# Kernel tuning notes

Measured on AMD Instinct MI355X. Metric: run time of the kernel, lower is better.

Reference implementation:

```python
import jax, jax.numpy as jnp
import numpy as np

D_MODEL = 1024
SEL_DIM = 64
CONFIGS = [(4, 32), (8, 64), (16, 128)]  # (heads, dim)
B, T = 2, 2048


def setup_inputs() -> dict:
    key = jax.random.key(0)
    ks = jax.random.split(key, 20)
    s = 0.02  # init scale for stability
    inp = {
        "x": jax.random.normal(ks[0], (B, T, D_MODEL), jnp.float32),
        "sel_w1": jax.random.normal(ks[1], (SEL_DIM, D_MODEL), jnp.float32) * s,
        "sel_b1": jnp.zeros((SEL_DIM,), jnp.float32),
        "sel_w2": jax.random.normal(ks[2], (SEL_DIM, SEL_DIM), jnp.float32) * s,
        "sel_b2": jnp.zeros((SEL_DIM,), jnp.float32),
        "sel_w3": jax.random.normal(ks[3], (len(CONFIGS), SEL_DIM), jnp.float32) * s,
        "sel_b3": jnp.zeros((len(CONFIGS),), jnp.float32),
    }
    for i, (h, d) in enumerate(CONFIGS):
        inp[f"qw{i}"] = jax.random.normal(ks[4 + 3 * i], (h * d, D_MODEL), jnp.float32) * s
        inp[f"kw{i}"] = jax.random.normal(ks[5 + 3 * i], (d, D_MODEL), jnp.float32) * s
        inp[f"ww{i}"] = jax.random.normal(ks[6 + 3 * i], (h, D_MODEL), jnp.float32) * s
    return inp


def _seq_features(x):
    # x: [b,t,d]
    b, t, d = x.shape
    seq_mean = jnp.mean(x, axis=1, keepdims=True)            # [b,1,d]
    seq_std = jnp.std(x, axis=1, keepdims=True, ddof=1)      # torch.std is unbiased
    pos = (jnp.arange(t, dtype=x.dtype) / t)[None, :, None]  # [1,t,1] broadcast to [b,t,d]
    return x + seq_mean + seq_std + pos * 0.1


def _forward(x, sel_w1, sel_b1, sel_w2, sel_b2, sel_w3, sel_b3,
             qw0, kw0, ww0, qw1, kw1, ww1, qw2, kw2, ww2):
    b, t, dm = x.shape
    feats = _seq_features(x)
    h1 = jax.nn.relu(feats @ sel_w1.T + sel_b1)
    h2 = jax.nn.relu(h1 @ sel_w2.T + sel_b2)
    config_probs = jax.nn.softmax(h2 @ sel_w3.T + sel_b3, axis=-1)  # [b,t,ncfg]

    per_cfg = [(qw0, kw0, ww0), (qw1, kw1, ww1), (qw2, kw2, ww2)]
    final = jnp.zeros((b, t, t), dtype=x.dtype)
    for i, ((heads, dim), (qw, kw, ww)) in enumerate(zip(CONFIGS, per_cfg)):
        q = (x @ qw.T).reshape(b, t, heads, dim)   # [b,t,h,d]
        k = x @ kw.T                               # [b,s,d]
        w = x @ ww.T                               # [b,t,h]
        dots = jnp.einsum('bthd,bsd->bths', q, k)  # [b,t,h,s]
        score = jnp.einsum('bths,bth->bts', jax.nn.relu(dots), w)  # relu*weight, sum heads
        final = final + config_probs[:, :, i:i + 1] * score
    return final


def reference(x, sel_w1, sel_b1, sel_w2, sel_b2, sel_w3, sel_b3,
              qw0, kw0, ww0, qw1, kw1, ww1, qw2, kw2, ww2):
    return _forward(x, sel_w1, sel_b1, sel_w2, sel_b2, sel_w3, sel_b3,
                    qw0, kw0, ww0, qw1, kw1, ww1, qw2, kw2, ww2)
```

## Files before the change

kernel.cpp:

```cpp
#include <hip/hip_runtime.h>
#include <hip/hip_fp16.h>
#include <cstdint>
#include <cstddef>
#include <math.h>

#define B_ 2
#define T_ 2048
#define D_ 1024
#define M_ (B_*T_)

#define QO0 0
#define KO0 128
#define WO0 160
#define QO1 168
#define KO1 680
#define WO1 744
#define QO2 752
#define KO2 2800
#define WO2 2928
#define SELO 2944
#define LDN 3072

typedef float f32x16 __attribute__((ext_vector_type(16)));
typedef short bf16x8 __attribute__((ext_vector_type(8)));
typedef unsigned short u16;

__device__ __forceinline__ u16 f2bf(float f) {
    unsigned int u = __float_as_uint(f);
    unsigned int r = (u + 0x7fffu + ((u >> 16) & 1u)) >> 16;
    return (u16)r;
}
__device__ __forceinline__ float bf2f(u16 b) {
    return __uint_as_float(((unsigned int)b) << 16);
}

__device__ __forceinline__ void gload16(const void* g, void* l) {
    __builtin_amdgcn_global_load_lds(
        (const __attribute__((address_space(1))) unsigned int*)g,
        (__attribute__((address_space(3))) unsigned int*)l,
        16, 0, 0);
}

__device__ __forceinline__ void stage_plane(const u16* src_base, int row_stride, int k0,
                                            int rg, int lane, u16* dst) {
    int rl  = lane >> 2;
    int row = rg * 16 + rl;
    int q   = (lane & 3) ^ (rl & 3) ^ ((rl >> 2) & 3);
    const u16* s = src_base + (size_t)row * row_stride + k0 + q * 8;
    gload16(s, dst + rg * 512);
}

__global__ void stats1(const float* __restrict__ x, float* __restrict__ part,
                       float* __restrict__ part2, u16* __restrict__ Xh) {
    int d  = blockIdx.x * 256 + threadIdx.x;
    int tc = blockIdx.y;
    int b  = blockIdx.z;
    size_t base = (size_t)b * T_ * D_ + (size_t)tc * 16 * D_ + d;
    float s = 0.f, s2 = 0.f;
#pragma unroll
    for (int t = 0; t < 16; ++t) {
        float v = x[base + (size_t)t * D_];
        s += v; s2 += v * v;
        Xh[base + (size_t)t * D_] = f2bf(v);
    }
    part [(b * 128 + tc) * D_ + d] = s;
    part2[(b * 128 + tc) * D_ + d] = s2;
}

__global__ void stats2(const float* __restrict__ part, const float* __restrict__ part2,
                       const float* __restrict__ w1,
                       float* __restrict__ msd, float* __restrict__ s1) {
    __shared__ float msL[1024];
    __shared__ float ps[64][17];
    __shared__ float pw[64][17];
    int b = blockIdx.x, tid = threadIdx.x;
    float s = 0.f, s2 = 0.f;
#pragma unroll 8
    for (int i = 0; i < 128; ++i) {
        s  += part [(b * 128 + i) * D_ + tid];
        s2 += part2[(b * 128 + i) * D_ + tid];
    }
    float mean = s / (float)T_;
    float var  = (s2 - (float)T_ * mean * mean) / (float)(T_ - 1);
    msL[tid] = mean + sqrtf(fmaxf(var, 0.f));
    __syncthreads();
    int j = tid >> 4, cc = tid & 15;
    float am = 0.f, aw = 0.f;
    const float* wr = w1 + (size_t)j * D_ + cc * 64;
    const float* mr = msL + cc * 64;
    for (int dd = 0; dd < 64; ++dd) { float w = wr[dd]; am += mr[dd] * w; aw += w; }
    ps[j][cc] = am; pw[j][cc] = aw;
    __syncthreads();
    if (tid < 64) {
        float sm = 0.f, sw = 0.f;
        for (int i = 0; i < 16; ++i) { sm += ps[tid][i]; sw += pw[tid][i]; }
        msd[b * 64 + tid] = sm;
        if (b == 0) s1[tid] = sw;
    }
}

__global__ void split_w(const float* __restrict__ qw0, const float* __restrict__ kw0,
                        const float* __restrict__ ww0, const float* __restrict__ qw1,
                        const float* __restrict__ kw1, const float* __restrict__ ww1,
                        const float* __restrict__ qw2, const float* __restrict__ kw2,
                        const float* __restrict__ ww2, const float* __restrict__ w1s,
                        u16* __restrict__ Wh) {
    int row = blockIdx.x;
    int col = threadIdx.x * 4;
    const float* src = nullptr;
    if      (row < 128)  src = qw0 + (size_t)row * D_;
    else if (row < 160)  src = kw0 + (size_t)(row - 128) * D_;
    else if (row < 164)  src = ww0 + (size_t)(row - 160) * D_;
    else if (row < 168)  src = nullptr;
    else if (row < 680)  src = qw1 + (size_t)(row - 168) * D_;
    else if (row < 744)  src = kw1 + (size_t)(row - 680) * D_;
    else if (row < 752)  src = ww1 + (size_t)(row - 744) * D_;
    else if (row < 2800) src = qw2 + (size_t)(row - 752) * D_;
    else if (row < 2928) src = kw2 + (size_t)(row - 2800) * D_;
    else if (row < 2944) src = ww2 + (size_t)(row - 2928) * D_;
    else if (row < 3008) src = w1s + (size_t)(row - 2944) * D_;
    float4 v = src ? *(const float4*)(src + col) : make_float4(0.f, 0.f, 0.f, 0.f);
    ushort4 h;
    h.x = f2bf(v.x); h.y = f2bf(v.y); h.z = f2bf(v.z); h.w = f2bf(v.w);
    *(ushort4*)&Wh[(size_t)row * D_ + col] = h;
}

__global__ __launch_bounds__(256, 3) void proj_gemm(
    const u16* __restrict__ Xh, const u16* __restrict__ Wh, u16* __restrict__ Ph) {
    __shared__ u16 As[8192], Bs[8192];
    int tid = threadIdx.x;
    int wave = tid >> 6, lane = tid & 63;
    int bm = blockIdx.x * 128, bn = blockIdx.y * 128;
    int wt = wave >> 1, wn = wave & 1;
    int fm = lane & 31, hv = lane >> 5;
    int tkey = (fm & 3) ^ ((fm >> 2) & 3);
    f32x16 acc[2][2];
#pragma unroll
    for (int i = 0; i < 2; ++i)
#pragma unroll
        for (int j = 0; j < 2; ++j)
#pragma unroll
            for (int r = 0; r < 16; ++r) acc[i][j][r] = 0.f;

    const u16* xh = Xh + (size_t)bm * D_;
    const u16* wh = Wh + (size_t)bn * D_;

    for (int kc = 0; kc < 16; ++kc) {
        int k0 = kc * 64;
#pragma unroll
        for (int i = 0; i < 8; ++i) {
            int j = wave * 8 + i;
            int mat = j >> 4;
            int pl  = (j >> 3) & 1;
            int rg  = j & 7;
            stage_plane(mat ? wh : xh, D_, k0 + pl * 32, rg, lane,
                        (mat ? Bs : As) + pl * 4096);
        }
        __syncthreads();
#pragma unroll
        for (int ks = 0; ks < 4; ++ks) {
            int pl = ks >> 1;
            int slot8 = (((ks & 1) * 2 + hv) ^ tkey) * 8;
            bf16x8 a_h[2], b_h[2];
#pragma unroll
            for (int t = 0; t < 2; ++t) {
                a_h[t] = *(const bf16x8*)&As[pl * 4096 + (wt * 64 + t * 32 + fm) * 32 + slot8];
                b_h[t] = *(const bf16x8*)&Bs[pl * 4096 + (wn * 64 + t * 32 + fm) * 32 + slot8];
            }
#pragma unroll
            for (int ti = 0; ti < 2; ++ti)
#pragma unroll
                for (int tj = 0; tj < 2; ++tj)
                    acc[ti][tj] = __builtin_amdgcn_mfma_f32_32x32x16_bf16(a_h[ti], b_h[tj], acc[ti][tj], 0, 0, 0);
        }
        __syncthreads();
    }
#pragma unroll
    for (int ti = 0; ti < 2; ++ti)
#pragma unroll
        for (int tj = 0; tj < 2; ++tj)
#pragma unroll
            for (int r = 0; r < 16; ++r) {
                int row = bm + wt * 64 + ti * 32 + (r & 3) + 8 * (r >> 2) + 4 * hv;
                int col = bn + wn * 64 + tj * 32 + fm;
                Ph[(size_t)row * LDN + col] = f2bf(acc[ti][tj][r]);
            }
}

__global__ void selector2(const u16* __restrict__ Ph,
                          const float* __restrict__ msd, const float* __restrict__ s1,
                          const float* __restrict__ b1, const float* __restrict__ w2,
                          const float* __restrict__ b2, const float* __restrict__ w3,
                          const float* __restrict__ b3, __half* __restrict__ WP) {
    __shared__ float h1s[4][64];
    __shared__ float h2s[4][64];
    __shared__ float lg[4][3];
    int tid = threadIdx.x;
    int slot = tid >> 6, j = tid & 63;
    int bt = blockIdx.x * 4 + slot;
    int b = bt >> 11, t = bt & 2047;
    size_t pidx = (size_t)bt * LDN + SELO + j;
    float v = bf2f(Ph[pidx])
            + msd[b * 64 + j] + 0.1f * ((float)t / (float)T_) * s1[j] + b1[j];
    h1s[slot][j] = fmaxf(v, 0.f);
    __syncthreads();
    float a2 = b2[j];
#pragma unroll 8
    for (int d = 0; d < 64; ++d) a2 = fmaf(h1s[slot][d], w2[j * 64 + d], a2);
    h2s[slot][j] = fmaxf(a2, 0.f);
    __syncthreads();
    if (j < 3) {
        float a3 = b3[j];
        for (int d = 0; d < 64; ++d) a3 = fmaf(h2s[slot][d], w3[j * 64 + d], a3);
        lg[slot][j] = a3;
    }
    __syncthreads();
    if (j < 28) {
        float m = fmaxf(lg[slot][0], fmaxf(lg[slot][1], lg[slot][2]));
        float e0 = expf(lg[slot][0] - m), e1 = expf(lg[slot][1] - m), e2 = expf(lg[slot][2] - m);
        float inv = 1.f / (e0 + e1 + e2);
        int wcol = (j < 4) ? (WO0 + j) : ((j < 12) ? (WO1 + j - 4) : (WO2 + j - 12));
        float p = ((j < 4) ? e0 : ((j < 12) ? e1 : e2)) * inv;
        float w = bf2f(Ph[(size_t)bt * LDN + wcol]);
        WP[(size_t)(b * 28 + j) * T_ + t] = __float2half(w * p);
    }
}

__device__ __forceinline__ int qcol_of(int c) {
    if (c < 2)  return QO0 + c * 64;
    if (c < 10) return QO1 + (c - 2) * 64;
    return QO2 + (c - 10) * 64;
}

__global__ __launch_bounds__(256, 2) void score_kernel(
    const u16* __restrict__ Ph, const __half* __restrict__ WP, float* __restrict__ out) {
    __shared__ u16 Qs[2][8192];
    __shared__ u16 Ks[4 * 4096];
    __shared__ __half wpL[3584];
    int tid = threadIdx.x;
    int wave = tid >> 6, lane = tid & 63;
    int wt = wave >> 1, wn = wave & 1;
    int fm = lane & 31, hv = lane >> 5;
    int tkey = (fm & 3) ^ ((fm >> 2) & 3);

    int n = blockIdx.z * 256 + blockIdx.y * 16 + blockIdx.x;
    int p = (n & 7) * 4 + (n >> 7);
    int xb = (n >> 3) & 15;
    int b = p >> 4, yb = p & 15;
    int t0 = yb * 128, s0 = xb * 128;

    const u16* Pq = Ph + (size_t)(b * T_ + t0) * LDN;
    const u16* Pk = Ph + (size_t)(b * T_ + s0) * LDN;

    auto stageQ = [&](int buf, int qcol) {
#pragma unroll
        for (int i = 0; i < 4; ++i) {
            int j = (wave << 2) + i;
            int pl = j >> 3, rg = j & 7;
            stage_plane(Pq, LDN, qcol + pl * 32, rg, lane, &Qs[buf][pl * 4096]);
        }
    };

#pragma unroll
    for (int i = 0; i < 6; ++i) {
        int j = i * 4 + wave;
        int pl = j >> 3, rg = j & 7;
        int col = (pl == 0) ? KO0 : ((pl == 1) ? KO1 : KO1 + 32);
        stage_plane(Pk, LDN, col, rg, lane, &Ks[pl * 4096]);
    }
#pragma unroll
    for (int i = 0; i < 2; ++i) {
        int j = i * 4 + wave;
        if (j < 7) {
            const __half* src = WP + (size_t)(b * 28 + j * 4 + (lane >> 4)) * T_ + t0 + (lane & 15) * 8;
            gload16(src, (u16*)wpL + j * 512);
        }
    }
    stageQ(0, QO0);

    f32x16 outacc[2][2], dots[2][2], Z16;
#pragma unroll
    for (int r = 0; r < 16; ++r) Z16[r] = 0.f;
#pragma unroll
    for (int i = 0; i < 2; ++i)
#pragma unroll
        for (int j = 0; j < 2; ++j)
#pragma unroll
            for (int r = 0; r < 16; ++r) { outacc[i][j][r] = 0.f; dots[i][j][r] = 0.f; }

    auto epi = [&](int g) {
#pragma unroll
        for (int ti = 0; ti < 2; ++ti) {
            int rowbase = wt * 64 + ti * 32 + 4 * hv;
#pragma unroll
            for (int rq = 0; rq < 4; ++rq) {
                const __half2* wp2 = (const __half2*)&wpL[g * 128 + rowbase + rq * 8];
                float2 f01 = __half22float2(wp2[0]);
                float2 f23 = __half22float2(wp2[1]);
                float wv[4] = {f01.x, f01.y, f23.x, f23.y};
#pragma unroll
                for (int tj = 0; tj < 2; ++tj)
#pragma unroll
                    for (int r2 = 0; r2 < 4; ++r2) {
                        int r = rq * 4 + r2;
                        outacc[ti][tj][r] += fmaxf(dots[ti][tj][r], 0.f) * wv[r2];
                    }
            }
        }
    };

    auto phase64 = [&](const u16* qb, int kpA, int kpB, bool z0, bool midBreak,
                       int gMid, bool hasEnd, int gEnd) {
#pragma unroll
        for (int ks = 0; ks < 4; ++ks) {
            int kp = (ks < 2) ? kpA : kpB;
            int slot8 = (((ks & 1) * 2 + hv) ^ tkey) * 8;
            bool zero = (ks == 0 && z0) || (ks == 2 && midBreak);
            bf16x8 kf[2], qf[2];
#pragma unroll
            for (int tj = 0; tj < 2; ++tj)
                kf[tj] = *(const bf16x8*)&Ks[kp * 4096 + (wn * 64 + tj * 32 + fm) * 32 + slot8];
#pragma unroll
            for (int ti = 0; ti < 2; ++ti)
                qf[ti] = *(const bf16x8*)&qb[(ks >> 1) * 4096 + (wt * 64 + ti * 32 + fm) * 32 + slot8];
#pragma unroll
            for (int ti = 0; ti < 2; ++ti)
#pragma unroll
                for (int tj = 0; tj < 2; ++tj)
                    dots[ti][tj] = __builtin_amdgcn_mfma_f32_32x32x16_bf16(
                        qf[ti], kf[tj], zero ? Z16 : dots[ti][tj], 0, 0, 0);
            if (ks == 1 && midBreak) epi(gMid);
            if (ks == 3 && hasEnd)   epi(gEnd);
        }
    };

#pragma unroll
    for (int c = 0; c < 2; ++c) {
        __syncthreads();
        stageQ((c + 1) & 1, qcol_of(c + 1));
        phase64(Qs[c & 1], 0, 0, true, true, 2 * c, true, 2 * c + 1);
    }
    for (int h = 0; h < 8; ++h) {
        int c = 2 + h;
        __syncthreads();
        stageQ((c + 1) & 1, qcol_of(c + 1));
        phase64(Qs[c & 1], 1, 2, true, false, -1, true, 4 + h);
        if (h == 7) {
            __syncthreads();
            for (int j = wave; j < 32; j += 4) {
                int pl = j >> 3, rg = j & 7;
                stage_plane(Pk, LDN, KO2 + pl * 32, rg, lane, &Ks[pl * 4096]);
            }
        }
    }
    for (int h = 0; h < 16; ++h) {
        int c = 10 + 2 * h;
        __syncthreads();
        stageQ((c + 1) & 1, qcol_of(c + 1));
        phase64(Qs[c & 1], 0, 1, true, false, -1, false, -1);
        __syncthreads();
        if (c + 1 < 41) stageQ(c & 1, qcol_of(c + 2));
        phase64(Qs[(c + 1) & 1], 2, 3, false, false, -1, true, 12 + h);
    }

#pragma unroll
    for (int ti = 0; ti < 2; ++ti)
#pragma unroll
        for (int tj = 0; tj < 2; ++tj)
#pragma unroll
            for (int r = 0; r < 16; ++r) {
                int trow = wt * 64 + ti * 32 + (r & 3) + 8 * (r >> 2) + 4 * hv;
                int scol = wn * 64 + tj * 32 + fm;
                out[(size_t)(b * T_ + t0 + trow) * T_ + (s0 + scol)] = outacc[ti][tj][r];
            }
}

extern "C" void kernel_launch(void* const* d_in, const int* in_sizes, int n_in,
                              void* d_out, int out_size, void* d_ws, size_t ws_size,
                              hipStream_t stream) {
    const float* x   = (const float*)d_in[0];
    const float* w1  = (const float*)d_in[1];
    const float* b1  = (const float*)d_in[2];
    const float* w2  = (const float*)d_in[3];
    const float* b2  = (const float*)d_in[4];
    const float* w3  = (const float*)d_in[5];
    const float* b3  = (const float*)d_in[6];
    const float* qw0 = (const float*)d_in[7];
    const float* kw0 = (const float*)d_in[8];
    const float* ww0 = (const float*)d_in[9];
    const float* qw1 = (const float*)d_in[10];
    const float* kw1 = (const float*)d_in[11];
    const float* ww1 = (const float*)d_in[12];
    const float* qw2 = (const float*)d_in[13];
    const float* kw2 = (const float*)d_in[14];
    const float* ww2 = (const float*)d_in[15];
    float* out = (float*)d_out;

    float* fb = (float*)d_ws;
    float* PA  = fb; fb += (size_t)B_ * 128 * D_;
    float* PA2 = fb; fb += (size_t)B_ * 128 * D_;
    float* MSD = fb; fb += 128;
    float* S1  = fb; fb += 64;
    __half* WP = (__half*)fb; fb += (size_t)B_ * 28 * T_ / 2;
    u16* ub = (u16*)fb;
    u16* Wh = ub; ub += (size_t)LDN * D_;
    u16* Xh = ub; ub += (size_t)M_ * D_;
    u16* Ph = ub; ub += (size_t)M_ * LDN;

    stats1<<<dim3(D_ / 256, 128, B_), 256, 0, stream>>>(x, PA, PA2, Xh);
    stats2<<<dim3(B_), 1024, 0, stream>>>(PA, PA2, w1, MSD, S1);
    split_w<<<dim3(LDN), 256, 0, stream>>>(qw0, kw0, ww0, qw1, kw1, ww1,
                                           qw2, kw2, ww2, w1, Wh);
    proj_gemm<<<dim3(M_ / 128, LDN / 128), 256, 0, stream>>>(Xh, Wh, Ph);
    selector2<<<dim3(M_ / 4), 256, 0, stream>>>(Ph, MSD, S1, b1, w2, b2, w3, b3, WP);
    score_kernel<<<dim3(T_ / 128, T_ / 128, B_), 256, 0, stream>>>(Ph, WP, out);
}
```

Before: 256.8 us.

## Register-resident K fragments with 128x64 score tiles, split stats2 across blocks

The score kernel now uses 128x64 output tiles instead of 128x128, so each wave owns a 32x64 strip. The K fragments for each config are loaded once into registers rather than re-read from LDS on every step. LDS is unified into one buffer and launch bounds rise to 3 blocks per CU, with 1024 blocks launched. The single-block stats2 reduction is split into two wider parallel kernels (column reduction, then a shuffle-based dot with w1) to remove a serial bottleneck. The trade-offs are higher register pressure, twice as many Q loads per output, and one extra kernel launch.

```diff
diff --git a/kernel.cpp b/kernel.cpp
--- a/kernel.cpp
+++ b/kernel.cpp
@@ -67,35 +67,50 @@
     part2[(b * 128 + tc) * D_ + d] = s2;
 }
 
-__global__ void stats2(const float* __restrict__ part, const float* __restrict__ part2,
-                       const float* __restrict__ w1,
-                       float* __restrict__ msd, float* __restrict__ s1) {
-    __shared__ float msL[1024];
-    __shared__ float ps[64][17];
-    __shared__ float pw[64][17];
-    int b = blockIdx.x, tid = threadIdx.x;
+__global__ void stats2a(const float* __restrict__ part, const float* __restrict__ part2,
+                        float* __restrict__ MS) {
+    __shared__ float r1[4][64], r2[4][64];
+    int blk = blockIdx.x;
+    int b = blk >> 4, dg = blk & 15;
+    int tid = threadIdx.x;
+    int dl = tid & 63, sl = tid >> 6;
+    int d = dg * 64 + dl;
     float s = 0.f, s2 = 0.f;
-#pragma unroll 8
-    for (int i = 0; i < 128; ++i) {
-        s  += part [(b * 128 + i) * D_ + tid];
-        s2 += part2[(b * 128 + i) * D_ + tid];
-    }
-    float mean = s / (float)T_;
-    float var  = (s2 - (float)T_ * mean * mean) / (float)(T_ - 1);
-    msL[tid] = mean + sqrtf(fmaxf(var, 0.f));
-    __syncthreads();
-    int j = tid >> 4, cc = tid & 15;
-    float am = 0.f, aw = 0.f;
-    const float* wr = w1 + (size_t)j * D_ + cc * 64;
-    const float* mr = msL + cc * 64;
-    for (int dd = 0; dd < 64; ++dd) { float w = wr[dd]; am += mr[dd] * w; aw += w; }
-    ps[j][cc] = am; pw[j][cc] = aw;
-    __syncthreads();
-    if (tid < 64) {
-        float sm = 0.f, sw = 0.f;
-        for (int i = 0; i < 16; ++i) { sm += ps[tid][i]; sw += pw[tid][i]; }
-        msd[b * 64 + tid] = sm;
-        if (b == 0) s1[tid] = sw;
+    for (int i = sl; i < 128; i += 4) {
+        s  += part [(b * 128 + i) * D_ + d];
+        s2 += part2[(b * 128 + i) * D_ + d];
+    }
+    r1[sl][dl] = s; r2[sl][dl] = s2;
+    __syncthreads();
+    if (sl == 0) {
+        s  = r1[0][dl] + r1[1][dl] + r1[2][dl] + r1[3][dl];
+        s2 = r2[0][dl] + r2[1][dl] + r2[2][dl] + r2[3][dl];
+        float mean = s / (float)T_;
+        float var  = (s2 - (float)T_ * mean * mean) / (float)(T_ - 1);
+        MS[b * D_ + d] = mean + sqrtf(fmaxf(var, 0.f));
+    }
+}
+
+__global__ void msdot(const float* __restrict__ MS, const float* __restrict__ w1,
+                      float* __restrict__ msd, float* __restrict__ s1) {
+    __shared__ float rA[4], rW[4];
+    int blk = blockIdx.x;
+    int b = blk >> 6, j = blk & 63;
+    int tid = threadIdx.x;
+    float4 m = *(const float4*)(MS + (size_t)b * D_ + tid * 4);
+    float4 w = *(const float4*)(w1 + (size_t)j * D_ + tid * 4);
+    float am = m.x * w.x + m.y * w.y + m.z * w.z + m.w * w.w;
+    float aw = w.x + w.y + w.z + w.w;
+    for (int off = 32; off; off >>= 1) {
+        am += __shfl_down(am, off);
+        aw += __shfl_down(aw, off);
+    }
+    int wv = tid >> 6, ln = tid & 63;
+    if (ln == 0) { rA[wv] = am; rW[wv] = aw; }
+    __syncthreads();
+    if (tid == 0) {
+        msd[b * 64 + j] = rA[0] + rA[1] + rA[2] + rA[3];
+        if (b == 0) s1[j] = rW[0] + rW[1] + rW[2] + rW[3];
     }
 }
 
@@ -232,22 +247,19 @@
     return QO2 + (c - 10) * 64;
 }
 
-__global__ __launch_bounds__(256, 2) void score_kernel(
+__global__ __launch_bounds__(256, 3) void score_kernel(
     const u16* __restrict__ Ph, const __half* __restrict__ WP, float* __restrict__ out) {
-    __shared__ u16 Qs[2][8192];
-    __shared__ u16 Ks[4 * 4096];
+    __shared__ u16 QsF[16384];
     __shared__ __half wpL[3584];
     int tid = threadIdx.x;
     int wave = tid >> 6, lane = tid & 63;
-    int wt = wave >> 1, wn = wave & 1;
     int fm = lane & 31, hv = lane >> 5;
     int tkey = (fm & 3) ^ ((fm >> 2) & 3);
 
-    int n = blockIdx.z * 256 + blockIdx.y * 16 + blockIdx.x;
-    int p = (n & 7) * 4 + (n >> 7);
-    int xb = (n >> 3) & 15;
-    int b = p >> 4, yb = p & 15;
-    int t0 = yb * 128, s0 = xb * 128;
+    int n = blockIdx.x;
+    int qt = (n & 7) * 4 + ((n >> 8) & 3);
+    int b = qt >> 4, t0 = (qt & 15) * 128;
+    int s0 = ((n >> 3) & 31) * 64;
 
     const u16* Pq = Ph + (size_t)(b * T_ + t0) * LDN;
     const u16* Pk = Ph + (size_t)(b * T_ + s0) * LDN;
@@ -255,18 +267,18 @@
     auto stageQ = [&](int buf, int qcol) {
 #pragma unroll
         for (int i = 0; i < 4; ++i) {
-            int j = (wave << 2) + i;
+            int j = wave * 4 + i;
             int pl = j >> 3, rg = j & 7;
-            stage_plane(Pq, LDN, qcol + pl * 32, rg, lane, &Qs[buf][pl * 4096]);
+            stage_plane(Pq, LDN, qcol + pl * 32, rg, lane, &QsF[buf * 8192 + pl * 4096]);
         }
     };
 
 #pragma unroll
-    for (int i = 0; i < 6; ++i) {
+    for (int i = 0; i < 3; ++i) {
         int j = i * 4 + wave;
-        int pl = j >> 3, rg = j & 7;
-        int col = (pl == 0) ? KO0 : ((pl == 1) ? KO1 : KO1 + 32);
-        stage_plane(Pk, LDN, col, rg, lane, &Ks[pl * 4096]);
+        int pl = j >> 2, rg = j & 3;
+        int col = (pl == 0) ? KO0 : ((pl == 1) ? KO1 : (KO1 + 32));
+        stage_plane(Pk, LDN, col, rg, lane, &QsF[pl * 2048]);
     }
 #pragma unroll
     for (int i = 0; i < 2; ++i) {
@@ -276,103 +288,156 @@
             gload16(src, (u16*)wpL + j * 512);
         }
     }
+    __syncthreads();
+    bf16x8 k0f[2][2], k1f[2][2][2];
+#pragma unroll
+    for (int h = 0; h < 2; ++h)
+#pragma unroll
+        for (int tj = 0; tj < 2; ++tj) {
+            int slot8 = ((h * 2 + hv) ^ tkey) * 8;
+            int ro = (tj * 32 + fm) * 32 + slot8;
+            k0f[h][tj]    = *(const bf16x8*)&QsF[ro];
+            k1f[0][h][tj] = *(const bf16x8*)&QsF[2048 + ro];
+            k1f[1][h][tj] = *(const bf16x8*)&QsF[4096 + ro];
+        }
+    __syncthreads();
     stageQ(0, QO0);
 
-    f32x16 outacc[2][2], dots[2][2], Z16;
+    f32x16 outacc[2], dots[2], Z16;
 #pragma unroll
     for (int r = 0; r < 16; ++r) Z16[r] = 0.f;
 #pragma unroll
-    for (int i = 0; i < 2; ++i)
-#pragma unroll
-        for (int j = 0; j < 2; ++j)
-#pragma unroll
-            for (int r = 0; r < 16; ++r) { outacc[i][j][r] = 0.f; dots[i][j][r] = 0.f; }
-
+    for (int tj = 0; tj < 2; ++tj)
+#pragma unroll
+        for (int r = 0; r < 16; ++r) { outacc[tj][r] = 0.f; dots[tj][r] = 0.f; }
+
+    auto qread = [&](const u16* qb, int pl, int half) -> bf16x8 {
+        int slot8 = ((half * 2 + hv) ^ tkey) * 8;
+        return *(const bf16x8*)&qb[pl * 4096 + (wave * 32 + fm) * 32 + slot8];
+    };
     auto epi = [&](int g) {
-#pragma unroll
-        for (int ti = 0; ti < 2; ++ti) {
-            int rowbase = wt * 64 + ti * 32 + 4 * hv;
-#pragma unroll
-            for (int rq = 0; rq < 4; ++rq) {
-                const __half2* wp2 = (const __half2*)&wpL[g * 128 + rowbase + rq * 8];
-                float2 f01 = __half22float2(wp2[0]);
-                float2 f23 = __half22float2(wp2[1]);
-                float wv[4] = {f01.x, f01.y, f23.x, f23.y};
-#pragma unroll
-                for (int tj = 0; tj < 2; ++tj)
-#pragma unroll
-                    for (int r2 = 0; r2 < 4; ++r2) {
-                        int r = rq * 4 + r2;
-                        outacc[ti][tj][r] += fmaxf(dots[ti][tj][r], 0.f) * wv[r2];
-                    }
-            }
+        int rowbase = wave * 32 + 4 * hv;
+#pragma unroll
+        for (int rq = 0; rq < 4; ++rq) {
+            const __half2* wp2 = (const __half2*)&wpL[g * 128 + rowbase + rq * 8];
+            float2 f01 = __half22float2(wp2[0]);
+            float2 f23 = __half22float2(wp2[1]);
+            float wv[4] = {f01.x, f01.y, f23.x, f23.y};
+#pragma unroll
+            for (int tj = 0; tj < 2; ++tj)
+#pragma unroll
+                for (int r2 = 0; r2 < 4; ++r2) {
+                    int r = rq * 4 + r2;
+                    outacc[tj][r] += fmaxf(dots[tj][r], 0.f) * wv[r2];
+                }
         }
     };
 
-    auto phase64 = [&](const u16* qb, int kpA, int kpB, bool z0, bool midBreak,
-                       int gMid, bool hasEnd, int gEnd) {
-#pragma unroll
-        for (int ks = 0; ks < 4; ++ks) {
-            int kp = (ks < 2) ? kpA : kpB;
-            int slot8 = (((ks & 1) * 2 + hv) ^ tkey) * 8;
-            bool zero = (ks == 0 && z0) || (ks == 2 && midBreak);
-            bf16x8 kf[2], qf[2];
-#pragma unroll
-            for (int tj = 0; tj < 2; ++tj)
-                kf[tj] = *(const bf16x8*)&Ks[kp * 4096 + (wn * 64 + tj * 32 + fm) * 32 + slot8];
-#pragma unroll
-            for (int ti = 0; ti < 2; ++ti)
-                qf[ti] = *(const bf16x8*)&qb[(ks >> 1) * 4096 + (wt * 64 + ti * 32 + fm) * 32 + slot8];
-#pragma unroll
-            for (int ti = 0; ti < 2; ++ti)
-#pragma unroll
-                for (int tj = 0; tj < 2; ++tj)
-                    dots[ti][tj] = __builtin_amdgcn_mfma_f32_32x32x16_bf16(
-                        qf[ti], kf[tj], zero ? Z16 : dots[ti][tj], 0, 0, 0);
-            if (ks == 1 && midBreak) epi(gMid);
-            if (ks == 3 && hasEnd)   epi(gEnd);
-        }
-    };
-
 #pragma unroll
     for (int c = 0; c < 2; ++c) {
         __syncthreads();
         stageQ((c + 1) & 1, qcol_of(c + 1));
-        phase64(Qs[c & 1], 0, 0, true, true, 2 * c, true, 2 * c + 1);
+        const u16* qb = &QsF[(c & 1) * 8192];
+        bf16x8 q;
+        q = qread(qb, 0, 0);
+        dots[0] = __builtin_amdgcn_mfma_f32_32x32x16_bf16(q, k0f[0][0], Z16, 0, 0, 0);
+        dots[1] = __builtin_amdgcn_mfma_f32_32x32x16_bf16(q, k0f[0][1], Z16, 0, 0, 0);
+        q = qread(qb, 0, 1);
+        dots[0] = __builtin_amdgcn_mfma_f32_32x32x16_bf16(q, k0f[1][0], dots[0], 0, 0, 0);
+        dots[1] = __builtin_amdgcn_mfma_f32_32x32x16_bf16(q, k0f[1][1], dots[1], 0, 0, 0);
+        epi(2 * c);
+        q = qread(qb, 1, 0);
+        dots[0] = __builtin_amdgcn_mfma_f32_32x32x16_bf16(q, k0f[0][0], Z16, 0, 0, 0);
+        dots[1] = __builtin_amdgcn_mfma_f32_32x32x16_bf16(q, k0f[0][1], Z16, 0, 0, 0);
+        q = qread(qb, 1, 1);
+        dots[0] = __builtin_amdgcn_mfma_f32_32x32x16_bf16(q, k0f[1][0], dots[0], 0, 0, 0);
+        dots[1] = __builtin_amdgcn_mfma_f32_32x32x16_bf16(q, k0f[1][1], dots[1], 0, 0, 0);
+        epi(2 * c + 1);
     }
     for (int h = 0; h < 8; ++h) {
         int c = 2 + h;
         __syncthreads();
-        stageQ((c + 1) & 1, qcol_of(c + 1));
-        phase64(Qs[c & 1], 1, 2, true, false, -1, true, 4 + h);
-        if (h == 7) {
-            __syncthreads();
-            for (int j = wave; j < 32; j += 4) {
-                int pl = j >> 3, rg = j & 7;
-                stage_plane(Pk, LDN, KO2 + pl * 32, rg, lane, &Ks[pl * 4096]);
+        if (c < 9) stageQ((c + 1) & 1, qcol_of(c + 1));
+        else {
+#pragma unroll
+            for (int i = 0; i < 4; ++i) {
+                int j = wave * 4 + i;
+                int pl = j >> 2, rg = j & 3;
+                stage_plane(Pk, LDN, KO2 + pl * 32, rg, lane, &QsF[pl * 2048]);
             }
         }
-    }
+        const u16* qb = &QsF[(c & 1) * 8192];
+        bf16x8 q;
+        q = qread(qb, 0, 0);
+        dots[0] = __builtin_amdgcn_mfma_f32_32x32x16_bf16(q, k1f[0][0][0], Z16, 0, 0, 0);
+        dots[1] = __builtin_amdgcn_mfma_f32_32x32x16_bf16(q, k1f[0][0][1], Z16, 0, 0, 0);
+        q = qread(qb, 0, 1);
+        dots[0] = __builtin_amdgcn_mfma_f32_32x32x16_bf16(q, k1f[0][1][0], dots[0], 0, 0, 0);
+        dots[1] = __builtin_amdgcn_mfma_f32_32x32x16_bf16(q, k1f[0][1][1], dots[1], 0, 0, 0);
+        q = qread(qb, 1, 0);
+        dots[0] = __builtin_amdgcn_mfma_f32_32x32x16_bf16(q, k1f[1][0][0], dots[0], 0, 0, 0);
+        dots[1] = __builtin_amdgcn_mfma_f32_32x32x16_bf16(q, k1f[1][0][1], dots[1], 0, 0, 0);
+        q = qread(qb, 1, 1);
+        dots[0] = __builtin_amdgcn_mfma_f32_32x32x16_bf16(q, k1f[1][1][0], dots[0], 0, 0, 0);
+        dots[1] = __builtin_amdgcn_mfma_f32_32x32x16_bf16(q, k1f[1][1][1], dots[1], 0, 0, 0);
+        epi(4 + h);
+    }
+    __syncthreads();
+    bf16x8 k2f[4][2][2];
+#pragma unroll
+    for (int p = 0; p < 4; ++p)
+#pragma unroll
+        for (int h = 0; h < 2; ++h)
+#pragma unroll
+            for (int tj = 0; tj < 2; ++tj) {
+                int slot8 = ((h * 2 + hv) ^ tkey) * 8;
+                k2f[p][h][tj] = *(const bf16x8*)&QsF[p * 2048 + (tj * 32 + fm) * 32 + slot8];
+            }
+    __syncthreads();
+    stageQ(0, qcol_of(10));
     for (int h = 0; h < 16; ++h) {
         int c = 10 + 2 * h;
         __syncthreads();
-        stageQ((c + 1) & 1, qcol_of(c + 1));
-        phase64(Qs[c & 1], 0, 1, true, false, -1, false, -1);
-        __syncthreads();
-        if (c + 1 < 41) stageQ(c & 1, qcol_of(c + 2));
-        phase64(Qs[(c + 1) & 1], 2, 3, false, false, -1, true, 12 + h);
-    }
-
-#pragma unroll
-    for (int ti = 0; ti < 2; ++ti)
-#pragma unroll
-        for (int tj = 0; tj < 2; ++tj)
-#pragma unroll
-            for (int r = 0; r < 16; ++r) {
-                int trow = wt * 64 + ti * 32 + (r & 3) + 8 * (r >> 2) + 4 * hv;
-                int scol = wn * 64 + tj * 32 + fm;
-                out[(size_t)(b * T_ + t0 + trow) * T_ + (s0 + scol)] = outacc[ti][tj][r];
-            }
+        stageQ(1, qcol_of(c + 1));
+        const u16* qb = &QsF[0];
+        bf16x8 q;
+        q = qread(qb, 0, 0);
+        dots[0] = __builtin_amdgcn_mfma_f32_32x32x16_bf16(q, k2f[0][0][0], Z16, 0, 0, 0);
+        dots[1] = __builtin_amdgcn_mfma_f32_32x32x16_bf16(q, k2f[0][0][1], Z16, 0, 0, 0);
+        q = qread(qb, 0, 1);
+        dots[0] = __builtin_amdgcn_mfma_f32_32x32x16_bf16(q, k2f[0][1][0], dots[0], 0, 0, 0);
+        dots[1] = __builtin_amdgcn_mfma_f32_32x32x16_bf16(q, k2f[0][1][1], dots[1], 0, 0, 0);
+        q = qread(qb, 1, 0);
+        dots[0] = __builtin_amdgcn_mfma_f32_32x32x16_bf16(q, k2f[1][0][0], dots[0], 0, 0, 0);
+        dots[1] = __builtin_amdgcn_mfma_f32_32x32x16_bf16(q, k2f[1][0][1], dots[1], 0, 0, 0);
+        q = qread(qb, 1, 1);
+        dots[0] = __builtin_amdgcn_mfma_f32_32x32x16_bf16(q, k2f[1][1][0], dots[0], 0, 0, 0);
+        dots[1] = __builtin_amdgcn_mfma_f32_32x32x16_bf16(q, k2f[1][1][1], dots[1], 0, 0, 0);
+        __syncthreads();
+        if (h < 15) stageQ(0, qcol_of(c + 2));
+        const u16* qc = &QsF[8192];
+        q = qread(qc, 0, 0);
+        dots[0] = __builtin_amdgcn_mfma_f32_32x32x16_bf16(q, k2f[2][0][0], dots[0], 0, 0, 0);
+        dots[1] = __builtin_amdgcn_mfma_f32_32x32x16_bf16(q, k2f[2][0][1], dots[1], 0, 0, 0);
+        q = qread(qc, 0, 1);
+        dots[0] = __builtin_amdgcn_mfma_f32_32x32x16_bf16(q, k2f[2][1][0], dots[0], 0, 0, 0);
+        dots[1] = __builtin_amdgcn_mfma_f32_32x32x16_bf16(q, k2f[2][1][1], dots[1], 0, 0, 0);
+        q = qread(qc, 1, 0);
+        dots[0] = __builtin_amdgcn_mfma_f32_32x32x16_bf16(q, k2f[3][0][0], dots[0], 0, 0, 0);
+        dots[1] = __builtin_amdgcn_mfma_f32_32x32x16_bf16(q, k2f[3][0][1], dots[1], 0, 0, 0);
+        q = qread(qc, 1, 1);
+        dots[0] = __builtin_amdgcn_mfma_f32_32x32x16_bf16(q, k2f[3][1][0], dots[0], 0, 0, 0);
+        dots[1] = __builtin_amdgcn_mfma_f32_32x32x16_bf16(q, k2f[3][1][1], dots[1], 0, 0, 0);
+        epi(12 + h);
+    }
+
+#pragma unroll
+    for (int tj = 0; tj < 2; ++tj)
+#pragma unroll
+        for (int r = 0; r < 16; ++r) {
+            int trow = wave * 32 + (r & 3) + 8 * (r >> 2) + 4 * hv;
+            out[(size_t)(b * T_ + t0 + trow) * T_ + s0 + tj * 32 + fm] = outacc[tj][r];
+        }
 }
 
 extern "C" void kernel_launch(void* const* d_in, const int* in_sizes, int n_in,
@@ -399,6 +464,7 @@
     float* fb = (float*)d_ws;
     float* PA  = fb; fb += (size_t)B_ * 128 * D_;
     float* PA2 = fb; fb += (size_t)B_ * 128 * D_;
+    float* MS  = fb; fb += (size_t)B_ * D_;
     float* MSD = fb; fb += 128;
     float* S1  = fb; fb += 64;
     __half* WP = (__half*)fb; fb += (size_t)B_ * 28 * T_ / 2;
@@ -408,10 +474,11 @@
     u16* Ph = ub; ub += (size_t)M_ * LDN;
 
     stats1<<<dim3(D_ / 256, 128, B_), 256, 0, stream>>>(x, PA, PA2, Xh);
-    stats2<<<dim3(B_), 1024, 0, stream>>>(PA, PA2, w1, MSD, S1);
+    stats2a<<<dim3(B_ * 16), 256, 0, stream>>>(PA, PA2, MS);
+    msdot<<<dim3(B_ * 64), 256, 0, stream>>>(MS, w1, MSD, S1);
     split_w<<<dim3(LDN), 256, 0, stream>>>(qw0, kw0, ww0, qw1, kw1, ww1,
                                            qw2, kw2, ww2, w1, Wh);
     proj_gemm<<<dim3(M_ / 128, LDN / 128), 256, 0, stream>>>(Xh, Wh, Ph);
     selector2<<<dim3(M_ / 4), 256, 0, stream>>>(Ph, MSD, S1, b1, w2, b2, w3, b3, WP);
-    score_kernel<<<dim3(T_ / 128, T_ / 128, B_), 256, 0, stream>>>(Ph, WP, out);
-}
+    score_kernel<<<dim3(1024), 256, 0, stream>>>(Ph, WP, out);
+}
```

Result: slower. 264.4 us (+3.0%).
